# Kernel tuning notes

Measured on AMD Instinct MI355X. Metric: run time of the kernel, lower is better.

The kernel has to match this reference:

```python
import jax, jax.numpy as jnp
import numpy as np

B, S, D_IN = 2, 2048, 2048
H, KVH, HD = 32, 8, 64
GROUPS = H // KVH
EPS = 1e-6
SCALE = HD ** -0.5


def setup_inputs() -> dict:
    key = jax.random.key(0)
    ks = jax.random.split(key, 6)
    x = jax.random.normal(ks[0], (B, S, D_IN), jnp.float32)
    Wq = jax.random.normal(ks[1], (H * HD, D_IN), jnp.float32) * 0.02
    Wk = jax.random.normal(ks[2], (KVH * HD, D_IN), jnp.float32) * 0.02
    Wv = jax.random.normal(ks[3], (KVH * HD, D_IN), jnp.float32) * 0.02
    Wo = jax.random.normal(ks[4], (D_IN, H * HD), jnp.float32) * 0.02
    w_qnorm = jnp.ones((HD,), jnp.float32)
    w_knorm = jnp.ones((HD,), jnp.float32)
    # Llama-style RoPE tables: [S, HD] with frequencies duplicated across halves
    inv_freq = 1.0 / (10000.0 ** (np.arange(0, HD, 2, dtype=np.float32) / HD))
    ang = np.outer(np.arange(S, dtype=np.float32), inv_freq)  # [S, HD/2]
    emb = np.concatenate([ang, ang], axis=-1)  # [S, HD]
    cos = jnp.asarray(np.cos(emb), jnp.float32)
    sin = jnp.asarray(np.sin(emb), jnp.float32)
    mask = jnp.tril(jnp.ones((S, S), jnp.bool_))  # unused by module (causal hardcoded)
    return dict(x=x, mask=mask, cos=cos, sin=sin, Wq=Wq, Wk=Wk, Wv=Wv, Wo=Wo,
                w_qnorm=w_qnorm, w_knorm=w_knorm)


def _rms_norm(t, w):
    # per-head-dim RMSNorm, eps inside sqrt (torch nn.RMSNorm semantics)
    var = jnp.mean(jnp.square(t), axis=-1, keepdims=True)
    return t * jax.lax.rsqrt(var + EPS) * w


def _rotate_half(t):
    t1, t2 = jnp.split(t, 2, axis=-1)
    return jnp.concatenate([-t2, t1], axis=-1)


def _rope(t, cos, sin):
    # t: [B,H,S,HD]; cos/sin: [S,HD]
    return t * cos[None, None] + _rotate_half(t) * sin[None, None]


def reference(x, mask, cos, sin, Wq, Wk, Wv, Wo, w_qnorm, w_knorm):
    bs, seq, _ = x.shape
    q = (x @ Wq.T).reshape(bs, seq, H, HD).transpose(0, 2, 1, 3)    # [B,H,S,hd]
    k = (x @ Wk.T).reshape(bs, seq, KVH, HD).transpose(0, 2, 1, 3)  # [B,KVH,S,hd]
    v = (x @ Wv.T).reshape(bs, seq, KVH, HD).transpose(0, 2, 1, 3)
    # GQA: repeat_interleave KV over head dim
    k = jnp.repeat(k, GROUPS, axis=1)
    v = jnp.repeat(v, GROUPS, axis=1)
    # fused QK RMSNorm then RoPE
    q = _rope(_rms_norm(q, w_qnorm), cos, sin)
    k = _rope(_rms_norm(k, w_knorm), cos, sin)
    # causal attention
    scores = jnp.einsum('bhqd,bhkd->bhqk', q, k) * SCALE
    causal = jnp.arange(seq)[:, None] >= jnp.arange(seq)[None, :]
    scores = jnp.where(causal, scores, jnp.finfo(scores.dtype).min)
    attn = jax.nn.softmax(scores, axis=-1)
    out = jnp.einsum('bhqk,bhkd->bhqd', attn, v)
    out = out.transpose(0, 2, 1, 3).reshape(bs, seq, H * HD)
    return out @ Wo.T
```

## Files before the change

### kernel.cpp

```cpp
#include <hip/hip_runtime.h>

typedef __bf16 bf16_t;
typedef __bf16 bf16x8 __attribute__((ext_vector_type(8)));
typedef __bf16 bf16x4 __attribute__((ext_vector_type(4)));
typedef float f32x4 __attribute__((ext_vector_type(4)));
typedef unsigned int u32;

#define AS1 __attribute__((address_space(1)))
#define AS3 __attribute__((address_space(3)))

#define ASTR 72

#if __has_builtin(__builtin_amdgcn_exp2f)
#define EXP2(x) __builtin_amdgcn_exp2f(x)
#else
#define EXP2(x) exp2f(x)
#endif

__device__ __forceinline__ void g2l16(const bf16_t* g, bf16_t* l) {
  __builtin_amdgcn_global_load_lds((const AS1 u32*)g, (AS3 u32*)l, 16, 0, 0);
}

__device__ __forceinline__ u32 pkbf(float a, float b) {
  u32 ua = __builtin_bit_cast(u32, a) + 0x8000u;
  u32 ub = __builtin_bit_cast(u32, b) + 0x8000u;
  return (ua >> 16) | (ub & 0xFFFF0000u);
}

__global__ __launch_bounds__(256) void cvt5(
    const float* __restrict__ s0, const float* __restrict__ s1,
    const float* __restrict__ s2, const float* __restrict__ s3,
    const float* __restrict__ s4,
    bf16_t* __restrict__ d0, bf16_t* __restrict__ d1, bf16_t* __restrict__ d2,
    bf16_t* __restrict__ d3, bf16_t* __restrict__ d4)
{
  int blk = blockIdx.x;
  const float* s; bf16_t* d; int off;
  if      (blk <  8192) { s = s0; d = d0; off = blk;         }
  else if (blk < 12288) { s = s1; d = d1; off = blk -  8192; }
  else if (blk < 13312) { s = s2; d = d2; off = blk - 12288; }
  else if (blk < 14336) { s = s3; d = d3; off = blk - 13312; }
  else                  { s = s4; d = d4; off = blk - 14336; }
  size_t i = (size_t)off * 1024 + threadIdx.x * 4;
  float4 v = *(const float4*)&s[i];
  bf16x4 t;
  t[0] = (bf16_t)v.x; t[1] = (bf16_t)v.y; t[2] = (bf16_t)v.z; t[3] = (bf16_t)v.w;
  *(bf16x4*)&d[i] = t;
}

__device__ __forceinline__ void gemm_core(
    const bf16_t* __restrict__ A, const bf16_t* __restrict__ B, int K,
    bf16_t* As0, bf16_t* As1, bf16_t* Bs0, bf16_t* Bs1, f32x4 (&acc)[4][4])
{
  const int tid = threadIdx.x, lane = tid & 63, w = tid >> 6;
  const int col = lane & 15, quad = lane >> 4;
  const int wm = w >> 1, wn = w & 1;
  const int lr = lane >> 2;
  const int lc = (((lane & 3) ^ ((lane >> 3) & 3)) << 3);
  const int sw = ((quad ^ ((col >> 1) & 3)) << 3);
  const bf16_t* ga = A + (size_t)(w * 16 + lr) * K + lc;
  const bf16_t* gb = B + (size_t)(w * 16 + lr) * K + lc;
  const int lo0 = (w * 16) * 32, lo1 = (64 + w * 16) * 32;

  g2l16(ga,                  As0 + lo0);
  g2l16(ga + (size_t)64 * K, As0 + lo1);
  g2l16(gb,                  Bs0 + lo0);
  g2l16(gb + (size_t)64 * K, Bs0 + lo1);

  const int nkb = K >> 5;
  for (int kb = 0; kb < nkb; ++kb) {
    __syncthreads();
    bf16_t* Ac = (kb & 1) ? As1 : As0;
    bf16_t* Bc = (kb & 1) ? Bs1 : Bs0;
    if (kb + 1 < nkb) {
      bf16_t* An = (kb & 1) ? As0 : As1;
      bf16_t* Bn = (kb & 1) ? Bs0 : Bs1;
      const int k2 = (kb + 1) * 32;
      g2l16(ga + k2,                  An + lo0);
      g2l16(ga + k2 + (size_t)64 * K, An + lo1);
      g2l16(gb + k2,                  Bn + lo0);
      g2l16(gb + k2 + (size_t)64 * K, Bn + lo1);
    }

    bf16x8 af[4], bfr[4];
#pragma unroll
    for (int mt = 0; mt < 4; ++mt)
      af[mt] = *(const bf16x8*)&Ac[(wm * 64 + mt * 16 + col) * 32 + sw];
#pragma unroll
    for (int nt = 0; nt < 4; ++nt)
      bfr[nt] = *(const bf16x8*)&Bc[(wn * 64 + nt * 16 + col) * 32 + sw];
#pragma unroll
    for (int mt = 0; mt < 4; ++mt)
#pragma unroll
      for (int nt = 0; nt < 4; ++nt)
        acc[mt][nt] = __builtin_amdgcn_mfma_f32_16x16x32_bf16(af[mt], bfr[nt], acc[mt][nt], 0, 0, 0);
  }
}

__global__ __launch_bounds__(256, 4) void gemm_qkv(
    const bf16_t* __restrict__ xb, const bf16_t* __restrict__ Wqb,
    const bf16_t* __restrict__ Wkb, const bf16_t* __restrict__ Wvb,
    const float* __restrict__ cosT, const float* __restrict__ sinT,
    const float* __restrict__ wq, const float* __restrict__ wk,
    bf16_t* __restrict__ Qn, bf16_t* __restrict__ Kn, bf16_t* __restrict__ Vt)
{
  __shared__ bf16_t S[16384];
  const int xcd = blockIdx.x & 7, c = blockIdx.x >> 3;
  const int bm = xcd * 4 + (c & 3), bn = c >> 2;
  const bf16_t* B;
  if      (bn < 16) B = Wqb + (size_t)bn * 128 * 2048;
  else if (bn < 20) B = Wkb + (size_t)(bn - 16) * 128 * 2048;
  else              B = Wvb + (size_t)(bn - 20) * 128 * 2048;

  f32x4 acc[4][4] = {};
  gemm_core(xb + (size_t)bm * 128 * 2048, B, 2048,
            &S[0], &S[4096], &S[8192], &S[12288], acc);

  const int lane = threadIdx.x & 63, w = threadIdx.x >> 6;
  const int col = lane & 15, quad = lane >> 4, wm = w >> 1, wn = w & 1;

  if (bn < 20) {
    const bool isQ = bn < 16;
    const float* wnv = isQ ? wq : wk;
    float w4[4];
#pragma unroll
    for (int nt = 0; nt < 4; ++nt) w4[nt] = wnv[nt * 16 + col];
    bf16_t* dst = isQ ? Qn + ((size_t)(bn * 2 + wn)) * 2048 * 64
                      : Kn + ((size_t)((bn - 16) * 2 + wn)) * 2048 * 64;
    const size_t bstride = isQ ? (size_t)32 * 2048 * 64 : (size_t)8 * 2048 * 64;
    const float qscale = 0.125f * 1.4426950408889634f;

#pragma unroll
    for (int mt = 0; mt < 4; ++mt)
#pragma unroll
      for (int r = 0; r < 4; ++r) {
        int row = bm * 128 + wm * 64 + mt * 16 + quad * 4 + r;
        int b = row >> 11, s = row & 2047;
        float v[4], ss = 0.f;
#pragma unroll
        for (int nt = 0; nt < 4; ++nt) { v[nt] = acc[mt][nt][r]; ss += v[nt] * v[nt]; }
        ss += __shfl_xor(ss, 1, 64);
        ss += __shfl_xor(ss, 2, 64);
        ss += __shfl_xor(ss, 4, 64);
        ss += __shfl_xor(ss, 8, 64);
        float rr = rsqrtf(ss * (1.0f / 64.0f) + 1e-6f);
        float t[4];
#pragma unroll
        for (int nt = 0; nt < 4; ++nt) t[nt] = v[nt] * rr * w4[nt];
        bf16_t* drow = dst + b * bstride + (size_t)s * 64;
#pragma unroll
        for (int nt = 0; nt < 4; ++nt) {
          int hd = nt * 16 + col;
          float rot = (nt < 2) ? -t[nt + 2] : t[nt - 2];
          float ov = t[nt] * cosT[s * 64 + hd] + rot * sinT[s * 64 + hd];
          if (isQ) ov *= qscale;
          drow[hd] = (bf16_t)ov;
        }
      }
  } else {
    const int vb = bn - 20;
    const int b = bm >> 4, s0 = (bm & 15) * 128;
    const int tid = threadIdx.x;
#pragma unroll
    for (int hh = 0; hh < 2; ++hh) {
      __syncthreads();
      if (wn == hh) {
#pragma unroll
        for (int mt = 0; mt < 4; ++mt)
#pragma unroll
          for (int nt = 0; nt < 4; ++nt)
#pragma unroll
            for (int r = 0; r < 4; ++r)
              S[(nt * 16 + col) * 136 + wm * 64 + mt * 16 + quad * 4 + r] =
                  (bf16_t)acc[mt][nt][r];
      }
      __syncthreads();
      const int kvh = vb * 2 + hh;
#pragma unroll
      for (int p = 0; p < 4; ++p) {
        int hd = p * 16 + (tid >> 4);
        int sc = (tid & 15) * 8;
        bf16x8 v = *(const bf16x8*)&S[hd * 136 + sc];
        *(bf16x8*)&Vt[((size_t)((b * 8 + kvh) * 64) + hd) * 2048 + s0 + sc] = v;
      }
    }
  }
}

__global__ __launch_bounds__(256, 4) void gemm_o(
    const bf16_t* __restrict__ Ao, const bf16_t* __restrict__ Wob,
    float* __restrict__ Cf)
{
  __shared__ bf16_t As[2][128 * 32], Bs[2][128 * 32];
  const int xcd = blockIdx.x & 7, c = blockIdx.x >> 3;
  const int bm = xcd * 4 + (c & 3), bn = c >> 2;
  f32x4 acc[4][4] = {};
  gemm_core(Ao + (size_t)bm * 128 * 2048, Wob + (size_t)bn * 128 * 2048, 2048,
            As[0], As[1], Bs[0], Bs[1], acc);

  const int lane = threadIdx.x & 63, w = threadIdx.x >> 6;
  const int col = lane & 15, quad = lane >> 4, wm = w >> 1, wn = w & 1;
#pragma unroll
  for (int mt = 0; mt < 4; ++mt)
#pragma unroll
    for (int r = 0; r < 4; ++r) {
      int row = bm * 128 + wm * 64 + mt * 16 + quad * 4 + r;
      float* crow = Cf + (size_t)row * 2048 + bn * 128 + wn * 64 + col;
#pragma unroll
      for (int nt = 0; nt < 4; ++nt)
        crow[nt * 16] = acc[mt][nt][r];
    }
}

__global__ __launch_bounds__(256, 3) void attn(
    const bf16_t* __restrict__ Qn, const bf16_t* __restrict__ Kn,
    const bf16_t* __restrict__ Vt, bf16_t* __restrict__ Ao)
{
  __shared__ bf16_t KsL[2][64 * 32], KsH[2][64 * 32];
  __shared__ bf16_t VsL[2][64 * 32], VsH[2][64 * 32];
  __shared__ bf16_t Ps[128 * ASTR];

  const int tid = threadIdx.x, lane = tid & 63, w = tid >> 6;
  const int col = lane & 15, quad = lane >> 4;
  const int lr = lane >> 2;
  const int lcs = (((lane & 3) ^ ((lane >> 3) & 3)) << 3);
  const int sw  = ((quad ^ ((col >> 1) & 3)) << 3);
  const int h = blockIdx.x, b = blockIdx.y;
  const int qt = 15 - blockIdx.z;
  const int kvh = h >> 2;

  const bf16_t* Kb = Kn + ((size_t)(b * 8 + kvh)) * 2048 * 64;
  const bf16_t* Vb = Vt + ((size_t)(b * 8 + kvh)) * 64 * 2048;
  const bf16_t* Qb = Qn + (((size_t)(b * 32 + h)) * 2048 + qt * 128) * 64;
  const int lw = w * 512;

  bf16x8 Qf[2][2];
#pragma unroll
  for (int mt = 0; mt < 2; ++mt)
#pragma unroll
    for (int kk = 0; kk < 2; ++kk)
      Qf[mt][kk] = *(const bf16x8*)&Qb[(w * 32 + mt * 16 + col) * 64 + kk * 32 + quad * 8];

  bf16x8 ones;
#pragma unroll
  for (int i = 0; i < 8; ++i) ones[i] = (bf16_t)1.0f;

  f32x4 o[2][4] = {};
  f32x4 lacc[2] = {};

  const int rowmin = qt * 128 + w * 32;
  const int rowmax = rowmin + 31;
  const int jmax = 2 * qt + 1;

  {
    const bf16_t* gk = &Kb[(size_t)(w * 16 + lr) * 64 + lcs];
    const bf16_t* gv = &Vb[(size_t)(w * 16 + lr) * 2048 + lcs];
    g2l16(gk,      &KsL[0][lw]);
    g2l16(gk + 32, &KsH[0][lw]);
    g2l16(gv,      &VsL[0][lw]);
    g2l16(gv + 32, &VsH[0][lw]);
  }

  for (int j = 0; j <= jmax; ++j) {
    __syncthreads();
    if (j < jmax) {
      const int nb = (j + 1) & 1;
      const bf16_t* gk = &Kb[(size_t)((j + 1) * 64 + w * 16 + lr) * 64 + lcs];
      const bf16_t* gv = &Vb[(size_t)(w * 16 + lr) * 2048 + (j + 1) * 64 + lcs];
      g2l16(gk,      &KsL[nb][lw]);
      g2l16(gk + 32, &KsH[nb][lw]);
      g2l16(gv,      &VsL[nb][lw]);
      g2l16(gv + 32, &VsH[nb][lw]);
    }

    if (j * 64 <= rowmax) {
      const int bf = j & 1;
      const bool needmask = (j * 64 + 63 > rowmin);

#pragma unroll
      for (int kt = 0; kt < 4; ++kt) {
        bf16x8 kf0 = *(const bf16x8*)&KsL[bf][(kt * 16 + col) * 32 + sw];
        bf16x8 kf1 = *(const bf16x8*)&KsH[bf][(kt * 16 + col) * 32 + sw];
        f32x4 st0 = {}, st1 = {};
        st0 = __builtin_amdgcn_mfma_f32_16x16x32_bf16(kf0, Qf[0][0], st0, 0, 0, 0);
        st0 = __builtin_amdgcn_mfma_f32_16x16x32_bf16(kf1, Qf[0][1], st0, 0, 0, 0);
        st1 = __builtin_amdgcn_mfma_f32_16x16x32_bf16(kf0, Qf[1][0], st1, 0, 0, 0);
        st1 = __builtin_amdgcn_mfma_f32_16x16x32_bf16(kf1, Qf[1][1], st1, 0, 0, 0);
        const int k0 = j * 64 + kt * 16 + quad * 4;
#pragma unroll
        for (int mt = 0; mt < 2; ++mt) {
          f32x4 st = mt ? st1 : st0;
          float p0 = EXP2(st[0]), p1 = EXP2(st[1]);
          float p2 = EXP2(st[2]), p3 = EXP2(st[3]);
          if (needmask) {
            const int qg = qt * 128 + w * 32 + mt * 16 + col;
            p0 = (k0 + 0 > qg) ? 0.f : p0;
            p1 = (k0 + 1 > qg) ? 0.f : p1;
            p2 = (k0 + 2 > qg) ? 0.f : p2;
            p3 = (k0 + 3 > qg) ? 0.f : p3;
          }
          uint2 pk = { pkbf(p0, p1), pkbf(p2, p3) };
          *(uint2*)&Ps[(w * 32 + mt * 16 + col) * ASTR + kt * 16 + quad * 4] = pk;
        }
      }
      asm volatile("s_waitcnt lgkmcnt(0)" ::: "memory");

#pragma unroll
      for (int kk = 0; kk < 2; ++kk) {
        const bf16_t* Vh = kk ? &VsH[bf][0] : &VsL[bf][0];
        bf16x8 pa0 = *(const bf16x8*)&Ps[(w * 32 + col) * ASTR + kk * 32 + quad * 8];
        bf16x8 pa1 = *(const bf16x8*)&Ps[(w * 32 + 16 + col) * ASTR + kk * 32 + quad * 8];
        lacc[0] = __builtin_amdgcn_mfma_f32_16x16x32_bf16(pa0, ones, lacc[0], 0, 0, 0);
        lacc[1] = __builtin_amdgcn_mfma_f32_16x16x32_bf16(pa1, ones, lacc[1], 0, 0, 0);
#pragma unroll
        for (int nt = 0; nt < 4; ++nt) {
          bf16x8 vf = *(const bf16x8*)&Vh[(nt * 16 + col) * 32 + sw];
          o[0][nt] = __builtin_amdgcn_mfma_f32_16x16x32_bf16(pa0, vf, o[0][nt], 0, 0, 0);
          o[1][nt] = __builtin_amdgcn_mfma_f32_16x16x32_bf16(pa1, vf, o[1][nt], 0, 0, 0);
        }
      }
    }
  }

#pragma unroll
  for (int mt = 0; mt < 2; ++mt)
#pragma unroll
    for (int r = 0; r < 4; ++r) {
      float inv = 1.0f / lacc[mt][r];
      int row = b * 2048 + qt * 128 + w * 32 + mt * 16 + quad * 4 + r;
      bf16_t* orow = &Ao[(size_t)row * 2048 + h * 64 + col];
#pragma unroll
      for (int nt = 0; nt < 4; ++nt)
        orow[nt * 16] = (bf16_t)(o[mt][nt][r] * inv);
    }
}

extern "C" void kernel_launch(void* const* d_in, const int* in_sizes, int n_in,
                              void* d_out, int out_size, void* d_ws, size_t ws_size,
                              hipStream_t stream)
{
  const float* x    = (const float*)d_in[0];
  const float* cosT = (const float*)d_in[2];
  const float* sinT = (const float*)d_in[3];
  const float* Wq   = (const float*)d_in[4];
  const float* Wk   = (const float*)d_in[5];
  const float* Wv   = (const float*)d_in[6];
  const float* Wo   = (const float*)d_in[7];
  const float* wq   = (const float*)d_in[8];
  const float* wk   = (const float*)d_in[9];
  float* out = (float*)d_out;

  char* ws = (char*)d_ws;
  bf16_t* xb  = (bf16_t*)(ws);
  bf16_t* Ao  = (bf16_t*)(ws);
  bf16_t* Wqb = (bf16_t*)(ws + 16777216);
  bf16_t* Wkb = (bf16_t*)(ws + 25165824);
  bf16_t* Wvb = (bf16_t*)(ws + 27262976);
  bf16_t* Wob = (bf16_t*)(ws + 29360128);
  bf16_t* Vt  = (bf16_t*)(ws + 37748736);
  bf16_t* Qn  = (bf16_t*)(ws + 41943040);
  bf16_t* Kn  = (bf16_t*)(ws + 58720256);

  cvt5<<<18432, 256, 0, stream>>>(x, Wq, Wk, Wv, Wo, xb, Wqb, Wkb, Wvb, Wob);
  gemm_qkv<<<768, 256, 0, stream>>>(xb, Wqb, Wkb, Wvb, cosT, sinT, wq, wk, Qn, Kn, Vt);
  attn<<<dim3(32, 2, 16), 256, 0, stream>>>(Qn, Kn, Vt, Ao);
  gemm_o<<<512, 256, 0, stream>>>(Ao, Wob, out);
}
```

Measured before the change: 288.5 us.

## Rewrite QKV projection as 256x256-tile 8-wave GEMM with deep LDS pipeline

```diff
diff --git a/kernel.cpp b/kernel.cpp
--- a/kernel.cpp
+++ b/kernel.cpp
@@ -97,48 +97,122 @@
   }
 }
 
-__global__ __launch_bounds__(256, 4) void gemm_qkv(
+#define ARG(s,k) (LS + ((s)*2+(k))*8192)
+#define BRG(s,k) (LS + 32768 + ((s)*2+(k))*8192)
+#define STG(rg, gp) do { \
+    g2l16((gp),                    (rg) + w*512); \
+    g2l16((gp) + (size_t)128*2048, (rg) + 4096 + w*512); } while(0)
+#define PH_LOADB(BR) \
+  _Pragma("unroll") for (int nf = 0; nf < 4; ++nf) \
+    bfr[nf] = *(const bf16x8*)&(BR)[(wn*64 + nf*16 + col)*32 + sw];
+#define PH_LOADA(AR, MH) \
+  _Pragma("unroll") for (int mf = 0; mf < 4; ++mf) \
+    af[mf] = *(const bf16x8*)&(AR)[(wm*128 + (MH)*64 + mf*16 + col)*32 + sw];
+#define PH_MID() \
+  __builtin_amdgcn_s_barrier(); \
+  asm volatile("s_waitcnt lgkmcnt(0)" ::: "memory"); \
+  __builtin_amdgcn_sched_barrier(0); \
+  __builtin_amdgcn_s_setprio(1)
+#define PH_MFMA(MH) \
+  _Pragma("unroll") for (int mf = 0; mf < 4; ++mf) \
+  _Pragma("unroll") for (int nf = 0; nf < 4; ++nf) \
+    acc[(MH)*4+mf][nf] = __builtin_amdgcn_mfma_f32_16x16x32_bf16(af[mf], bfr[nf], acc[(MH)*4+mf][nf], 0, 0, 0);
+#define PH_END() \
+  __builtin_amdgcn_s_setprio(0); \
+  __builtin_amdgcn_s_barrier()
+
+__global__ __launch_bounds__(512, 2) void gemm_qkv8(
     const bf16_t* __restrict__ xb, const bf16_t* __restrict__ Wqb,
     const bf16_t* __restrict__ Wkb, const bf16_t* __restrict__ Wvb,
     const float* __restrict__ cosT, const float* __restrict__ sinT,
     const float* __restrict__ wq, const float* __restrict__ wk,
     bf16_t* __restrict__ Qn, bf16_t* __restrict__ Kn, bf16_t* __restrict__ Vt)
 {
-  __shared__ bf16_t S[16384];
+  __shared__ bf16_t LS[65536];
+  const int tid = threadIdx.x, lane = tid & 63, w = tid >> 6;
+  const int col = lane & 15, quad = lane >> 4;
+  const int wm = w >> 2, wn = w & 3;
+  const int lr = lane >> 2;
+  const int lc = (((lane & 3) ^ ((lane >> 3) & 3)) << 3);
+  const int sw = ((quad ^ ((col >> 1) & 3)) << 3);
+
   const int xcd = blockIdx.x & 7, c = blockIdx.x >> 3;
-  const int bm = xcd * 4 + (c & 3), bn = c >> 2;
-  const bf16_t* B;
-  if      (bn < 16) B = Wqb + (size_t)bn * 128 * 2048;
-  else if (bn < 20) B = Wkb + (size_t)(bn - 16) * 128 * 2048;
-  else              B = Wvb + (size_t)(bn - 20) * 128 * 2048;
-
-  f32x4 acc[4][4] = {};
-  gemm_core(xb + (size_t)bm * 128 * 2048, B, 2048,
-            &S[0], &S[4096], &S[8192], &S[12288], acc);
-
-  const int lane = threadIdx.x & 63, w = threadIdx.x >> 6;
-  const int col = lane & 15, quad = lane >> 4, wm = w >> 1, wn = w & 1;
-
-  if (bn < 20) {
-    const bool isQ = bn < 16;
+  const int bm = xcd * 2 + c / 12, bn = c % 12;
+  const bf16_t* Bp;
+  if      (bn <  8) Bp = Wqb + (size_t)bn * 256 * 2048;
+  else if (bn < 10) Bp = Wkb + (size_t)(bn - 8) * 256 * 2048;
+  else              Bp = Wvb + (size_t)(bn - 10) * 256 * 2048;
+  const bf16_t* Ap = xb + (size_t)bm * 256 * 2048;
+
+  const bf16_t* ga = Ap + (size_t)(w * 16 + lr) * 2048 + lc;
+  const bf16_t* gb = Bp + (size_t)(w * 16 + lr) * 2048 + lc;
+
+  f32x4 acc[8][4] = {};
+  bf16x8 af[4], bfr[4];
+
+  STG(ARG(0,0), ga);        STG(BRG(0,0), gb);
+  STG(ARG(0,1), ga + 32);   STG(BRG(0,1), gb + 32);
+  STG(ARG(1,0), ga + 64);   STG(BRG(1,0), gb + 64);
+  asm volatile("s_waitcnt vmcnt(4)" ::: "memory");
+  __builtin_amdgcn_s_barrier();
+
+  for (int i = 0; i < 16; ++i) {
+    const int To = 2 * i + 1;
+    const int P2 = 2 * i + 2;
+    const bool pe = (i < 15);
+    PH_LOADB(BRG(0,0)); PH_LOADA(ARG(0,0), 0);
+    STG(ARG(1,1), ga + To * 64 + 32);
+    PH_MID(); PH_MFMA(0); PH_END();
+    PH_LOADA(ARG(0,0), 1);
+    STG(BRG(1,1), gb + To * 64 + 32);
+    PH_MID(); PH_MFMA(1); PH_END();
+    PH_LOADB(BRG(0,1)); PH_LOADA(ARG(0,1), 0);
+    if (pe) STG(ARG(0,0), ga + P2 * 64);
+    PH_MID(); PH_MFMA(0); PH_END();
+    PH_LOADA(ARG(0,1), 1);
+    if (pe) STG(BRG(0,0), gb + P2 * 64);
+    PH_MID(); PH_MFMA(1);
+    __builtin_amdgcn_s_setprio(0);
+    if (pe) { asm volatile("s_waitcnt vmcnt(4)" ::: "memory"); }
+    else    { asm volatile("s_waitcnt vmcnt(0)" ::: "memory"); }
+    __builtin_amdgcn_s_barrier();
+    PH_LOADB(BRG(1,0)); PH_LOADA(ARG(1,0), 0);
+    if (pe) STG(ARG(0,1), ga + P2 * 64 + 32);
+    PH_MID(); PH_MFMA(0); PH_END();
+    PH_LOADA(ARG(1,0), 1);
+    if (pe) STG(BRG(0,1), gb + P2 * 64 + 32);
+    PH_MID(); PH_MFMA(1); PH_END();
+    PH_LOADB(BRG(1,1)); PH_LOADA(ARG(1,1), 0);
+    if (pe) STG(ARG(1,0), ga + (P2 + 1) * 64);
+    PH_MID(); PH_MFMA(0); PH_END();
+    PH_LOADA(ARG(1,1), 1);
+    if (pe) STG(BRG(1,0), gb + (P2 + 1) * 64);
+    PH_MID(); PH_MFMA(1);
+    __builtin_amdgcn_s_setprio(0);
+    asm volatile("s_waitcnt vmcnt(4)" ::: "memory");
+    __builtin_amdgcn_s_barrier();
+  }
+
+  if (bn < 10) {
+    const bool isQ = bn < 8;
     const float* wnv = isQ ? wq : wk;
     float w4[4];
 #pragma unroll
-    for (int nt = 0; nt < 4; ++nt) w4[nt] = wnv[nt * 16 + col];
-    bf16_t* dst = isQ ? Qn + ((size_t)(bn * 2 + wn)) * 2048 * 64
-                      : Kn + ((size_t)((bn - 16) * 2 + wn)) * 2048 * 64;
+    for (int nf = 0; nf < 4; ++nf) w4[nf] = wnv[nf * 16 + col];
+    const int head = isQ ? bn * 4 + wn : (bn - 8) * 4 + wn;
+    bf16_t* dst = (isQ ? Qn : Kn) + (size_t)head * 2048 * 64;
     const size_t bstride = isQ ? (size_t)32 * 2048 * 64 : (size_t)8 * 2048 * 64;
     const float qscale = 0.125f * 1.4426950408889634f;
 
 #pragma unroll
-    for (int mt = 0; mt < 4; ++mt)
+    for (int mf = 0; mf < 8; ++mf)
 #pragma unroll
       for (int r = 0; r < 4; ++r) {
-        int row = bm * 128 + wm * 64 + mt * 16 + quad * 4 + r;
+        int row = bm * 256 + wm * 128 + mf * 16 + quad * 4 + r;
         int b = row >> 11, s = row & 2047;
         float v[4], ss = 0.f;
 #pragma unroll
-        for (int nt = 0; nt < 4; ++nt) { v[nt] = acc[mt][nt][r]; ss += v[nt] * v[nt]; }
+        for (int nf = 0; nf < 4; ++nf) { v[nf] = acc[mf][nf][r]; ss += v[nf] * v[nf]; }
         ss += __shfl_xor(ss, 1, 64);
         ss += __shfl_xor(ss, 2, 64);
         ss += __shfl_xor(ss, 4, 64);
@@ -146,42 +220,45 @@
         float rr = rsqrtf(ss * (1.0f / 64.0f) + 1e-6f);
         float t[4];
 #pragma unroll
-        for (int nt = 0; nt < 4; ++nt) t[nt] = v[nt] * rr * w4[nt];
+        for (int nf = 0; nf < 4; ++nf) t[nf] = v[nf] * rr * w4[nf];
         bf16_t* drow = dst + b * bstride + (size_t)s * 64;
 #pragma unroll
-        for (int nt = 0; nt < 4; ++nt) {
-          int hd = nt * 16 + col;
-          float rot = (nt < 2) ? -t[nt + 2] : t[nt - 2];
-          float ov = t[nt] * cosT[s * 64 + hd] + rot * sinT[s * 64 + hd];
+        for (int nf = 0; nf < 4; ++nf) {
+          int hd = nf * 16 + col;
+          float rot = (nf < 2) ? -t[nf + 2] : t[nf - 2];
+          float ov = t[nf] * cosT[s * 64 + hd] + rot * sinT[s * 64 + hd];
           if (isQ) ov *= qscale;
           drow[hd] = (bf16_t)ov;
         }
       }
   } else {
-    const int vb = bn - 20;
-    const int b = bm >> 4, s0 = (bm & 15) * 128;
-    const int tid = threadIdx.x;
+    const int b = bm >> 3;
+    const int kvb = bn - 10;
 #pragma unroll
     for (int hh = 0; hh < 2; ++hh) {
-      __syncthreads();
-      if (wn == hh) {
-#pragma unroll
-        for (int mt = 0; mt < 4; ++mt)
-#pragma unroll
-          for (int nt = 0; nt < 4; ++nt)
+      asm volatile("s_waitcnt lgkmcnt(0)" ::: "memory");
+      __builtin_amdgcn_s_barrier();
+      if (wm == hh) {
+#pragma unroll
+        for (int mf = 0; mf < 8; ++mf)
+#pragma unroll
+          for (int nf = 0; nf < 4; ++nf)
 #pragma unroll
             for (int r = 0; r < 4; ++r)
-              S[(nt * 16 + col) * 136 + wm * 64 + mt * 16 + quad * 4 + r] =
-                  (bf16_t)acc[mt][nt][r];
+              LS[wn * 8704 + (nf * 16 + col) * 136 + mf * 16 + quad * 4 + r] =
+                  (bf16_t)acc[mf][nf][r];
       }
-      __syncthreads();
-      const int kvh = vb * 2 + hh;
-#pragma unroll
-      for (int p = 0; p < 4; ++p) {
-        int hd = p * 16 + (tid >> 4);
-        int sc = (tid & 15) * 8;
-        bf16x8 v = *(const bf16x8*)&S[hd * 136 + sc];
-        *(bf16x8*)&Vt[((size_t)((b * 8 + kvh) * 64) + hd) * 2048 + s0 + sc] = v;
+      asm volatile("s_waitcnt lgkmcnt(0)" ::: "memory");
+      __builtin_amdgcn_s_barrier();
+      const int s0g = (bm & 7) * 256 + hh * 128;
+      const int tile = tid >> 7, r128 = tid & 127;
+      const int kvh = kvb * 4 + tile;
+#pragma unroll
+      for (int p = 0; p < 8; ++p) {
+        int hd = p * 8 + (r128 >> 4);
+        int sc = (r128 & 15) * 8;
+        bf16x8 v = *(const bf16x8*)&LS[tile * 8704 + hd * 136 + sc];
+        *(bf16x8*)&Vt[((size_t)((b * 8 + kvh) * 64) + hd) * 2048 + s0g + sc] = v;
       }
     }
   }
@@ -362,7 +439,7 @@
   bf16_t* Kn  = (bf16_t*)(ws + 58720256);
 
   cvt5<<<18432, 256, 0, stream>>>(x, Wq, Wk, Wv, Wo, xb, Wqb, Wkb, Wvb, Wob);
-  gemm_qkv<<<768, 256, 0, stream>>>(xb, Wqb, Wkb, Wvb, cosT, sinT, wq, wk, Qn, Kn, Vt);
+  gemm_qkv8<<<192, 512, 0, stream>>>(xb, Wqb, Wkb, Wvb, cosT, sinT, wq, wk, Qn, Kn, Vt);
   attn<<<dim3(32, 2, 16), 256, 0, stream>>>(Qn, Kn, Vt, Ao);
   gemm_o<<<512, 256, 0, stream>>>(Ao, Wob, out);
 }
```

Result: slower. 296.6 us (+2.8%).
